# Optimization experiments

Measured on AMD Instinct MI355X. Metric: run time of the kernel, lower is better.

## Reference

```python
import jax, jax.numpy as jnp
import numpy as np

EPS = 1e-12  # matches F.normalize default eps


def _l2norm(x, axis):
    n = jnp.sqrt(jnp.sum(x * x, axis=axis, keepdims=True))
    return x / jnp.maximum(n, EPS)


def setup_inputs() -> dict:
    key = jax.random.key(0)
    k1, k2 = jax.random.split(key)
    B, G, D, K = 512, 100, 768, 100
    h = jax.random.normal(k1, (B, G, D), dtype=jnp.float32)
    duplicate_pooling = jax.random.normal(k2, (G, D, K), dtype=jnp.float32)
    out_extrap = jnp.zeros((B, G, K), dtype=jnp.float32)
    return {"h": h, "duplicate_pooling": duplicate_pooling, "out_extrap": out_extrap}


def reference(h, duplicate_pooling, out_extrap):
    # Per-group: L2-normalize h_i over feature dim, L2-normalize w_i over its
    # first (feature) dim, then matmul. Fused across the group dim G.
    h_n = _l2norm(h, axis=-1)                       # [B, G, D]
    w_n = _l2norm(duplicate_pooling, axis=1)        # [G, D, K], normalize over D (dim=0 of each w_i)
    out = jnp.einsum("bgd,gdk->bgk", h_n, w_n)     # [B, G, K]
    return out
```

## Files before the change

kernel.cpp:

```cpp
#include <hip/hip_runtime.h>
#include <stdint.h>


#define G_   100
#define D_   768
#define K_   100
#define B_   512
#define KPAD 112
#define BM   64
#define BK   32
#define LDP  40

typedef __attribute__((ext_vector_type(8))) short bf16x8;
typedef __attribute__((ext_vector_type(4))) float f32x4;

__device__ __forceinline__ short f2bf(float f) {
    uint32_t u = __builtin_bit_cast(uint32_t, f);
    u = (u + 0x7FFFu + ((u >> 16) & 1u)) >> 16;
    return (short)u;
}

__global__ __launch_bounds__(256) void wnorm_part(const float* __restrict__ W,
                                                  float* __restrict__ wpart) {
    int bid = blockIdx.x;
    int g = bid / 6, dc = bid % 6;
    int t = threadIdx.x;
    int k = t & 127;
    float ss = 0.f;
    if (k < K_) {
        const float* p = W + ((size_t)(g * D_ + dc * 128 + (t >> 7))) * K_ + k;
        #pragma unroll 4
        for (int i = 0; i < 64; ++i) {
            float v = p[(size_t)(2 * i) * K_];
            ss += v * v;
        }
    }
    __shared__ float red[128];
    if (t < 128) red[t] = ss;
    __syncthreads();
    if (t >= 128) red[t - 128] += ss;
    __syncthreads();
    if (t < K_) wpart[(g * 6 + dc) * K_ + t] = red[t];
}

__global__ __launch_bounds__(256) void wprep(const float* __restrict__ W,
                                             const float* __restrict__ wpart,
                                             short* __restrict__ Wt) {
    int bid = blockIdx.x;
    int g = bid / 12, dc = bid % 12;
    int d0 = dc * 64;
    int t = threadIdx.x;
    __shared__ float tile[64][105];
    __shared__ float invn[K_];

    for (int s = t; s < 64 * 25; s += 256) {
        int d = s / 25, j = s % 25;
        const float4 v = *(const float4*)(W + ((size_t)(g * D_ + d0 + d)) * K_ + j * 4);
        tile[d][j * 4 + 0] = v.x; tile[d][j * 4 + 1] = v.y;
        tile[d][j * 4 + 2] = v.z; tile[d][j * 4 + 3] = v.w;
    }
    if (t < K_) {
        float ss = 0.f;
        #pragma unroll
        for (int c = 0; c < 6; ++c) ss += wpart[(g * 6 + c) * K_ + t];
        invn[t] = 1.f / fmaxf(sqrtf(ss), 1e-12f);
    }
    __syncthreads();

    for (int s = t; s < KPAD * 8; s += 256) {
        int k = s >> 3, j = s & 7;
        bf16x8 o;
        if (k < K_) {
            float inv = invn[k];
            #pragma unroll
            for (int i = 0; i < 8; ++i) o[i] = f2bf(tile[j * 8 + i][k] * inv);
        } else {
            #pragma unroll
            for (int i = 0; i < 8; ++i) o[i] = 0;
        }
        *(bf16x8*)(Wt + ((size_t)(g * KPAD + k)) * D_ + d0 + j * 8) = o;
    }
}

__global__ __launch_bounds__(256) void gemm(const float* __restrict__ h,
                                            const short* __restrict__ Wt,
                                            float* __restrict__ out) {
    int bid = blockIdx.x;
    int g = bid >> 3, mt = bid & 7;
    int b0 = mt * BM;
    int t = threadIdx.x;
    int wave = t >> 6, lane = t & 63;

    __shared__ __align__(16) short As[BM * LDP];
    __shared__ __align__(16) short Bs[KPAD * LDP];
    __shared__ float hss[BM];

    int ar = t >> 2, aq = t & 3;
    const float* hp = h + ((size_t)(b0 + ar) * G_ + g) * D_ + aq * 8;
    const short* wtg = Wt + (size_t)g * KPAD * D_;

    f32x4 acc[7];
    #pragma unroll
    for (int i = 0; i < 7; ++i) acc[i] = (f32x4){0.f, 0.f, 0.f, 0.f};
    float ss = 0.f;

    for (int kt = 0; kt < D_ / BK; ++kt) {
        __syncthreads();
        {
            const float* p = hp + kt * BK;
            float4 v0 = *(const float4*)(p);
            float4 v1 = *(const float4*)(p + 4);
            float vs[8] = {v0.x, v0.y, v0.z, v0.w, v1.x, v1.y, v1.z, v1.w};
            bf16x8 o;
            #pragma unroll
            for (int i = 0; i < 8; ++i) { ss += vs[i] * vs[i]; o[i] = f2bf(vs[i]); }
            *(bf16x8*)(As + ar * LDP + aq * 8) = o;
        }
        for (int s = t; s < KPAD * 4; s += 256) {
            int n = s >> 2, j = s & 3;
            bf16x8 v = *(const bf16x8*)(wtg + (size_t)n * D_ + kt * BK + j * 8);
            *(bf16x8*)(Bs + n * LDP + j * 8) = v;
        }
        __syncthreads();

        int frow = lane & 15, fk = (lane >> 4) * 8;
        bf16x8 a = *(const bf16x8*)(As + (wave * 16 + frow) * LDP + fk);
        #pragma unroll
        for (int nt = 0; nt < 7; ++nt) {
            bf16x8 b = *(const bf16x8*)(Bs + (nt * 16 + frow) * LDP + fk);
            acc[nt] = __builtin_amdgcn_mfma_f32_16x16x32_bf16(a, b, acc[nt], 0, 0, 0);
        }
    }

    ss += __shfl_xor(ss, 1);
    ss += __shfl_xor(ss, 2);
    if (aq == 0) hss[ar] = ss;
    __syncthreads();

    int col = lane & 15;
    int rbase = wave * 16 + (lane >> 4) * 4;
    float invh[4];
    #pragma unroll
    for (int r = 0; r < 4; ++r) invh[r] = 1.f / fmaxf(sqrtf(hss[rbase + r]), 1e-12f);
    #pragma unroll
    for (int nt = 0; nt < 7; ++nt) {
        int n = nt * 16 + col;
        if (n < K_) {
            #pragma unroll
            for (int r = 0; r < 4; ++r) {
                int b = b0 + rbase + r;
                out[((size_t)b * G_ + g) * K_ + n] = acc[nt][r] * invh[r];
            }
        }
    }
}

extern "C" void kernel_launch(void* const* d_in, const int* in_sizes, int n_in,
                              void* d_out, int out_size, void* d_ws, size_t ws_size,
                              hipStream_t stream) {
    const float* h = (const float*)d_in[0];
    const float* W = (const float*)d_in[1];
    float* out = (float*)d_out;

    short* Wt = (short*)d_ws;
    float* wpart = (float*)((char*)d_ws + (size_t)G_ * KPAD * D_ * 2);

    wnorm_part<<<dim3(G_ * 6),  dim3(256), 0, stream>>>(W, wpart);
    wprep     <<<dim3(G_ * 12), dim3(256), 0, stream>>>(W, wpart, Wt);
    gemm      <<<dim3(G_ * 8),  dim3(256), 0, stream>>>(h, Wt, out);
}
```

Baseline: 280.3 us.

## Fuse W norm into prep, double-buffer B via direct global-to-LDS loads

Removes the separate W-norm pass: wprep now writes unnormalized bf16 W and per-chunk sum of squares, and the GEMM epilogue applies the inverse column norm. The GEMM keeps the h fragment in registers instead of staging it in LDS. It double-buffers swizzled B tiles through global_load_lds with BK raised to 64, and prefetches the next h slice. Block-to-group mapping is reordered so neighbouring blocks share groups. This cuts one launch and one full read of W and overlaps loads with MFMA, at the cost of more registers and a padded 128-row W layout.

```diff
diff --git a/kernel.cpp b/kernel.cpp
--- a/kernel.cpp
+++ b/kernel.cpp
@@ -2,14 +2,15 @@
 #include <stdint.h>
 
 
-#define G_   100
-#define D_   768
-#define K_   100
-#define B_   512
-#define KPAD 112
-#define BM   64
-#define BK   32
-#define LDP  40
+#define G_    100
+#define D_    768
+#define K_    100
+#define B_    512
+#define KP_   128
+#define BM    64
+#define BK    64
+#define NT    7
+#define NITER (D_ / BK)
 
 typedef __attribute__((ext_vector_type(8))) short bf16x8;
 typedef __attribute__((ext_vector_type(4))) float f32x4;
@@ -20,38 +21,20 @@
     return (short)u;
 }
 
-__global__ __launch_bounds__(256) void wnorm_part(const float* __restrict__ W,
-                                                  float* __restrict__ wpart) {
-    int bid = blockIdx.x;
-    int g = bid / 6, dc = bid % 6;
-    int t = threadIdx.x;
-    int k = t & 127;
-    float ss = 0.f;
-    if (k < K_) {
-        const float* p = W + ((size_t)(g * D_ + dc * 128 + (t >> 7))) * K_ + k;
-        #pragma unroll 4
-        for (int i = 0; i < 64; ++i) {
-            float v = p[(size_t)(2 * i) * K_];
-            ss += v * v;
-        }
-    }
-    __shared__ float red[128];
-    if (t < 128) red[t] = ss;
-    __syncthreads();
-    if (t >= 128) red[t - 128] += ss;
-    __syncthreads();
-    if (t < K_) wpart[(g * 6 + dc) * K_ + t] = red[t];
+__device__ __forceinline__ void gl_lds16(const void* g, void* l) {
+    __builtin_amdgcn_global_load_lds(
+        (const __attribute__((address_space(1))) uint32_t*)g,
+        (__attribute__((address_space(3))) uint32_t*)l, 16, 0, 0);
 }
 
 __global__ __launch_bounds__(256) void wprep(const float* __restrict__ W,
-                                             const float* __restrict__ wpart,
-                                             short* __restrict__ Wt) {
+                                             short* __restrict__ Wt,
+                                             float* __restrict__ wpart) {
     int bid = blockIdx.x;
     int g = bid / 12, dc = bid % 12;
     int d0 = dc * 64;
     int t = threadIdx.x;
-    __shared__ float tile[64][105];
-    __shared__ float invn[K_];
+    __shared__ float tile[64][104];
 
     for (int s = t; s < 64 * 25; s += 256) {
         int d = s / 25, j = s % 25;
@@ -59,97 +42,137 @@
         tile[d][j * 4 + 0] = v.x; tile[d][j * 4 + 1] = v.y;
         tile[d][j * 4 + 2] = v.z; tile[d][j * 4 + 3] = v.w;
     }
-    if (t < K_) {
-        float ss = 0.f;
-        #pragma unroll
-        for (int c = 0; c < 6; ++c) ss += wpart[(g * 6 + c) * K_ + t];
-        invn[t] = 1.f / fmaxf(sqrtf(ss), 1e-12f);
-    }
     __syncthreads();
 
-    for (int s = t; s < KPAD * 8; s += 256) {
-        int k = s >> 3, j = s & 7;
-        bf16x8 o;
-        if (k < K_) {
-            float inv = invn[k];
+    int kp = t >> 1, h2 = t & 1;
+    float ss = 0.f;
+    short* dst = Wt + ((size_t)(g * KP_ + kp)) * D_ + d0 + h2 * 32;
+    if (kp < K_) {
+        #pragma unroll
+        for (int c = 0; c < 4; ++c) {
+            bf16x8 o;
             #pragma unroll
-            for (int i = 0; i < 8; ++i) o[i] = f2bf(tile[j * 8 + i][k] * inv);
-        } else {
-            #pragma unroll
-            for (int i = 0; i < 8; ++i) o[i] = 0;
+            for (int i = 0; i < 8; ++i) {
+                float v = tile[h2 * 32 + c * 8 + i][kp];
+                ss += v * v;
+                o[i] = f2bf(v);
+            }
+            *(bf16x8*)(dst + c * 8) = o;
         }
-        *(bf16x8*)(Wt + ((size_t)(g * KPAD + k)) * D_ + d0 + j * 8) = o;
+    } else {
+        bf16x8 z = {0, 0, 0, 0, 0, 0, 0, 0};
+        #pragma unroll
+        for (int c = 0; c < 4; ++c) *(bf16x8*)(dst + c * 8) = z;
     }
+    ss += __shfl_xor(ss, 1);
+    if (h2 == 0) wpart[(size_t)(g * 12 + dc) * KP_ + kp] = ss;
 }
 
 __global__ __launch_bounds__(256) void gemm(const float* __restrict__ h,
                                             const short* __restrict__ Wt,
+                                            const float* __restrict__ wpart,
                                             float* __restrict__ out) {
     int bid = blockIdx.x;
-    int g = bid >> 3, mt = bid & 7;
+    int g, mt;
+    if (bid < 768) { g = (bid & 7) + 8 * (bid >> 6); mt = (bid >> 3) & 7; }
+    else           { int l = bid - 768; g = 96 + (l & 3); mt = l >> 2; }
     int b0 = mt * BM;
     int t = threadIdx.x;
-    int wave = t >> 6, lane = t & 63;
+    int w = t >> 6, lane = t & 63;
+    int r = lane & 15, hh = lane >> 4;
 
-    __shared__ __align__(16) short As[BM * LDP];
-    __shared__ __align__(16) short Bs[KPAD * LDP];
+    __shared__ __align__(16) short Bs[2][KP_ * BK];
+    __shared__ float invw[KP_];
     __shared__ float hss[BM];
 
-    int ar = t >> 2, aq = t & 3;
-    const float* hp = h + ((size_t)(b0 + ar) * G_ + g) * D_ + aq * 8;
-    const short* wtg = Wt + (size_t)g * KPAD * D_;
+    const short* wtg = Wt + (size_t)g * KP_ * D_;
 
-    f32x4 acc[7];
+    if (t < KP_) {
+        float s2 = 0.f;
+        #pragma unroll
+        for (int c = 0; c < 12; ++c) s2 += wpart[(size_t)(g * 12 + c) * KP_ + t];
+        invw[t] = 1.f / fmaxf(sqrtf(s2), 1e-12f);
+    }
+
+    const float* hp = h + ((size_t)((b0 + w * 16 + r) * G_ + g)) * D_ + hh * 8;
+
+    auto stageB = [&](int kt, int p) {
+        char* base = (char*)&Bs[p][0];
+        #pragma unroll
+        for (int i = 0; i < 4; ++i) {
+            int c = w * 4 + i;
+            int kp = c * 8 + (lane >> 3);
+            int colb = (lane & 7) * 16;
+            int scol = colb ^ ((kp & 7) << 4);
+            const char* src = (const char*)(wtg + (size_t)kp * D_ + kt * BK) + scol;
+            gl_lds16(src, base + c * 1024);
+        }
+    };
+
+    f32x4 acc[NT];
     #pragma unroll
-    for (int i = 0; i < 7; ++i) acc[i] = (f32x4){0.f, 0.f, 0.f, 0.f};
+    for (int i = 0; i < NT; ++i) acc[i] = (f32x4){0.f, 0.f, 0.f, 0.f};
     float ss = 0.f;
 
-    for (int kt = 0; kt < D_ / BK; ++kt) {
-        __syncthreads();
-        {
-            const float* p = hp + kt * BK;
-            float4 v0 = *(const float4*)(p);
-            float4 v1 = *(const float4*)(p + 4);
-            float vs[8] = {v0.x, v0.y, v0.z, v0.w, v1.x, v1.y, v1.z, v1.w};
-            bf16x8 o;
-            #pragma unroll
-            for (int i = 0; i < 8; ++i) { ss += vs[i] * vs[i]; o[i] = f2bf(vs[i]); }
-            *(bf16x8*)(As + ar * LDP + aq * 8) = o;
-        }
-        for (int s = t; s < KPAD * 4; s += 256) {
-            int n = s >> 2, j = s & 3;
-            bf16x8 v = *(const bf16x8*)(wtg + (size_t)n * D_ + kt * BK + j * 8);
-            *(bf16x8*)(Bs + n * LDP + j * 8) = v;
-        }
+    stageB(0, 0);
+    float4 a00 = *(const float4*)(hp + 0);
+    float4 a01 = *(const float4*)(hp + 4);
+    float4 a10 = *(const float4*)(hp + 32);
+    float4 a11 = *(const float4*)(hp + 36);
+
+    for (int kt = 0; kt < NITER; ++kt) {
+        int p = kt & 1;
         __syncthreads();
 
-        int frow = lane & 15, fk = (lane >> 4) * 8;
-        bf16x8 a = *(const bf16x8*)(As + (wave * 16 + frow) * LDP + fk);
+        float4 n00 = {0,0,0,0}, n01 = {0,0,0,0}, n10 = {0,0,0,0}, n11 = {0,0,0,0};
+        if (kt + 1 < NITER) {
+            stageB(kt + 1, p ^ 1);
+            const float* np = hp + (kt + 1) * BK;
+            n00 = *(const float4*)(np + 0);
+            n01 = *(const float4*)(np + 4);
+            n10 = *(const float4*)(np + 32);
+            n11 = *(const float4*)(np + 36);
+        }
+
+        float av[16] = {a00.x, a00.y, a00.z, a00.w, a01.x, a01.y, a01.z, a01.w,
+                        a10.x, a10.y, a10.z, a10.w, a11.x, a11.y, a11.z, a11.w};
+        bf16x8 af0, af1;
         #pragma unroll
-        for (int nt = 0; nt < 7; ++nt) {
-            bf16x8 b = *(const bf16x8*)(Bs + (nt * 16 + frow) * LDP + fk);
-            acc[nt] = __builtin_amdgcn_mfma_f32_16x16x32_bf16(a, b, acc[nt], 0, 0, 0);
+        for (int i = 0; i < 8; ++i) { ss += av[i] * av[i];         af0[i] = f2bf(av[i]); }
+        #pragma unroll
+        for (int i = 0; i < 8; ++i) { ss += av[8 + i] * av[8 + i]; af1[i] = f2bf(av[8 + i]); }
+
+        const char* bb = (const char*)&Bs[p][0];
+        int swz = (r & 7) << 4;
+        #pragma unroll
+        for (int nt = 0; nt < NT; ++nt) {
+            int rowb = (nt * 16 + r) * 128;
+            bf16x8 bv0 = *(const bf16x8*)(bb + rowb + ((hh * 16) ^ swz));
+            bf16x8 bv1 = *(const bf16x8*)(bb + rowb + ((64 + hh * 16) ^ swz));
+            acc[nt] = __builtin_amdgcn_mfma_f32_16x16x32_bf16(af0, bv0, acc[nt], 0, 0, 0);
+            acc[nt] = __builtin_amdgcn_mfma_f32_16x16x32_bf16(af1, bv1, acc[nt], 0, 0, 0);
         }
+        a00 = n00; a01 = n01; a10 = n10; a11 = n11;
     }
 
-    ss += __shfl_xor(ss, 1);
-    ss += __shfl_xor(ss, 2);
-    if (aq == 0) hss[ar] = ss;
+    ss += __shfl_xor(ss, 16);
+    ss += __shfl_xor(ss, 32);
+    if (hh == 0) hss[w * 16 + r] = ss;
     __syncthreads();
 
-    int col = lane & 15;
-    int rbase = wave * 16 + (lane >> 4) * 4;
-    float invh[4];
+    int rbase = hh * 4;
+    float ih[4];
     #pragma unroll
-    for (int r = 0; r < 4; ++r) invh[r] = 1.f / fmaxf(sqrtf(hss[rbase + r]), 1e-12f);
+    for (int q = 0; q < 4; ++q) ih[q] = 1.f / fmaxf(sqrtf(hss[w * 16 + rbase + q]), 1e-12f);
     #pragma unroll
-    for (int nt = 0; nt < 7; ++nt) {
-        int n = nt * 16 + col;
+    for (int nt = 0; nt < NT; ++nt) {
+        int n = nt * 16 + r;
         if (n < K_) {
+            float iw = invw[n];
             #pragma unroll
-            for (int r = 0; r < 4; ++r) {
-                int b = b0 + rbase + r;
-                out[((size_t)b * G_ + g) * K_ + n] = acc[nt][r] * invh[r];
+            for (int q = 0; q < 4; ++q) {
+                int b = b0 + w * 16 + rbase + q;
+                out[((size_t)b * G_ + g) * K_ + n] = acc[nt][q] * iw * ih[q];
             }
         }
     }
@@ -162,10 +185,9 @@
     const float* W = (const float*)d_in[1];
     float* out = (float*)d_out;
 
-    short* Wt = (short*)d_ws;
-    float* wpart = (float*)((char*)d_ws + (size_t)G_ * KPAD * D_ * 2);
+    short* Wt    = (short*)d_ws;
+    float* wpart = (float*)((char*)d_ws + (size_t)G_ * KP_ * D_ * 2);
 
-    wnorm_part<<<dim3(G_ * 6),  dim3(256), 0, stream>>>(W, wpart);
-    wprep     <<<dim3(G_ * 12), dim3(256), 0, stream>>>(W, wpart, Wt);
-    gemm      <<<dim3(G_ * 8),  dim3(256), 0, stream>>>(h, Wt, out);
+    wprep<<<dim3(G_ * 12), dim3(256), 0, stream>>>(W, Wt, wpart);
+    gemm <<<dim3(G_ * 8),  dim3(256), 0, stream>>>(h, Wt, wpart, out);
 }
```

Measured after the change: 286.7 us. +2.3%, slower.
